# Kernel tuning notes

Hardware: AMD Instinct MI355X
Metric: run time of the kernel (lower is better)

Reference implementation:

```python
import jax, jax.numpy as jnp
import numpy as np

N_NODES = 50000
N_EDGES = 800000
DIM_IN = 128
DIM_H = 128
DIM_OUT = 8
N_GRAPHS = 32


def _glorot(key, shape):
    fan_in, fan_out = shape[0], shape[1]
    lim = float(np.sqrt(6.0 / (fan_in + fan_out)))
    return jax.random.uniform(key, shape, jnp.float32, -lim, lim)


def setup_inputs() -> dict:
    key = jax.random.key(0)
    ks = jax.random.split(key, 16)
    x = jax.random.normal(ks[0], (N_NODES, DIM_IN), jnp.float32)
    edge_index = jax.random.randint(ks[1], (2, N_EDGES), 0, N_NODES, jnp.int64)
    batch = jnp.sort(jax.random.randint(ks[2], (N_NODES,), 0, N_GRAPHS, jnp.int64))
    inp = {"x": x, "edge_index": edge_index, "batch": batch}
    # SAGEConv layers: lin_l (aggregated neighbors, with bias) + lin_r (self, no bias)
    dims = [(DIM_IN, DIM_H), (DIM_H, DIM_H), (DIM_H, DIM_H)]
    for i, (di, do) in enumerate(dims, start=1):
        inp[f"Wl{i}"] = _glorot(ks[2 + 3 * i], (di, do))
        inp[f"bl{i}"] = jnp.zeros((do,), jnp.float32)
        inp[f"Wr{i}"] = _glorot(ks[3 + 3 * i], (di, do))
    inp["W_lin1"] = _glorot(ks[13], (DIM_H, DIM_H))
    inp["b_lin1"] = jnp.zeros((DIM_H,), jnp.float32)
    inp["W_lin2"] = _glorot(ks[14], (DIM_H, DIM_OUT))
    inp["b_lin2"] = jnp.zeros((DIM_OUT,), jnp.float32)
    return inp


def _sage_conv(x, src, dst, Wl, bl, Wr):
    # mean aggregation of source-node features at destination nodes
    agg = jax.ops.segment_sum(x[src], dst, num_segments=N_NODES)
    cnt = jax.ops.segment_sum(jnp.ones((src.shape[0], 1), x.dtype), dst, num_segments=N_NODES)
    agg = agg / jnp.maximum(cnt, 1.0)
    return agg @ Wl + bl + x @ Wr


def reference(x, edge_index, batch, Wl1, bl1, Wr1, Wl2, bl2, Wr2, Wl3, bl3, Wr3,
              W_lin1, b_lin1, W_lin2, b_lin2):
    src, dst = edge_index[0], edge_index[1]
    h = jax.nn.relu(_sage_conv(x, src, dst, Wl1, bl1, Wr1))
    h = jax.nn.relu(_sage_conv(h, src, dst, Wl2, bl2, Wr2))
    h = jax.nn.relu(_sage_conv(h, src, dst, Wl3, bl3, Wr3))
    # global mean pool over graphs in the batch
    pooled = jax.ops.segment_sum(h, batch, num_segments=N_GRAPHS)
    gcnt = jax.ops.segment_sum(jnp.ones((h.shape[0], 1), h.dtype), batch, num_segments=N_GRAPHS)
    pooled = pooled / jnp.maximum(gcnt, 1.0)
    h = jax.nn.relu(pooled @ W_lin1 + b_lin1)
    # dropout p=0.5 is identity in eval mode
    return h @ W_lin2 + b_lin2
```

## Files before the change

kernel.cpp:

```cpp
#include <hip/hip_runtime.h>
#include <hip/hip_bf16.h>

#define N_NODES 50000
#define N_EDGES 800000
#define DIM 128
#define N_GRAPHS 32
#define POOL_ROWS 32
#define CAP 64
#define NPS 128
#define NSUP 391
#define SBCAP2 2432
#define EPB 8192
#define EPT 32
#define NBLK ((N_EDGES + EPB - 1) / EPB)

typedef _Float16 f16;
typedef __attribute__((ext_vector_type(2))) _Float16 f16x2;
typedef __attribute__((ext_vector_type(4))) _Float16 f16x4;
typedef __attribute__((ext_vector_type(8))) _Float16 f16x8;
typedef __attribute__((ext_vector_type(4))) float f32x4;

__global__ __launch_bounds__(256) void k_zero(float* __restrict__ pooled,
                                              int* __restrict__ gcnt,
                                              int* __restrict__ gCnt) {
  int i = blockIdx.x * 256 + threadIdx.x;
  if (i < N_GRAPHS * DIM) pooled[i] = 0.f;
  if (i < N_GRAPHS) gcnt[i] = 0;
  if (i < NSUP) gCnt[i] = 0;
}

__global__ __launch_bounds__(256) void k_part2(const int* __restrict__ src,
                                               const int* __restrict__ dst,
                                               int* __restrict__ gCnt,
                                               unsigned int* __restrict__ sbBuf) {
  __shared__ int hist[NSUP];
  __shared__ int base[NSUP];
  int tid = threadIdx.x;
  int e0 = blockIdx.x * EPB;
  int nE = min(EPB, N_EDGES - e0);
  for (int i = tid; i < NSUP; i += 256) hist[i] = 0;
  __syncthreads();
  unsigned pk[EPT];
  #pragma unroll
  for (int j = 0; j < EPT; ++j) {
    int idx = j * 256 + tid;
    if (idx < nE) {
      int e = e0 + idx;
      int d = dst[e], s = src[e];
      int sb = d >> 7;
      pk[j] = ((unsigned)sb << 23) | ((unsigned)(d & 127) << 16) | (unsigned)s;
      atomicAdd(&hist[sb], 1);
    } else pk[j] = 0xFFFFFFFFu;
  }
  __syncthreads();
  for (int i = tid; i < NSUP; i += 256) {
    int h = hist[i];
    base[i] = h ? atomicAdd(&gCnt[i], h) : 0;
    hist[i] = 0;
  }
  __syncthreads();
  #pragma unroll
  for (int j = 0; j < EPT; ++j) {
    unsigned p = pk[j];
    if (p != 0xFFFFFFFFu) {
      int sb = p >> 23;
      int slot = base[sb] + atomicAdd(&hist[sb], 1);
      if (slot < SBCAP2)
        sbBuf[(size_t)sb * SBCAP2 + slot] = p & 0x7FFFFFu;
    }
  }
}

__global__ __launch_bounds__(256) void k_bin(const int* __restrict__ gCnt,
                                             const unsigned int* __restrict__ sbBuf,
                                             int* __restrict__ cnt,
                                             unsigned short* __restrict__ esrc) {
  __shared__ unsigned short buck[NPS * CAP];
  __shared__ int cl[NPS];
  int sb = blockIdx.x, tid = threadIdx.x;
  for (int i = tid; i < NPS; i += 256) cl[i] = 0;
  __syncthreads();
  int n = min(gCnt[sb], SBCAP2);
  const unsigned int* buf = sbBuf + (size_t)sb * SBCAP2;
  for (int i = tid; i < n; i += 256) {
    unsigned p = buf[i];
    int dl = p >> 16;
    int slot = atomicAdd(&cl[dl], 1);
    if (slot < CAP) buck[dl * CAP + slot] = (unsigned short)(p & 0xFFFF);
  }
  __syncthreads();
  size_t basep = (size_t)sb * NPS * CAP;
  for (int i = tid; i < NPS * CAP; i += 256)
    esrc[basep + i] = buck[i];
  int n0 = sb * NPS;
  for (int d = tid; d < NPS; d += 256) {
    int node = n0 + d;
    if (node < N_NODES) cnt[node] = min(cl[d], CAP);
  }
}

__global__ void k_repack(const float* __restrict__ W0, const float* __restrict__ W1,
                         const float* __restrict__ W2, const float* __restrict__ W3,
                         const float* __restrict__ W4, const float* __restrict__ W5,
                         f16* __restrict__ pack) {
  int idx = blockIdx.x * 256 + threadIdx.x;
  if (idx >= 6 * 16384) return;
  int m = idx >> 14, r = idx & 16383;
  const float* W = m == 0 ? W0 : m == 1 ? W1 : m == 2 ? W2 : m == 3 ? W3 : m == 4 ? W4 : W5;
  int ct = r >> 11, ks = (r >> 9) & 3, l = (r >> 3) & 63, j = r & 7;
  int k = ks * 32 + ((l >> 4) << 3) + j;
  int c = ct * 16 + (l & 15);
  float w = W[k * DIM + c];
  f16 hi = (f16)w;
  f16 lo = (f16)(w - (float)hi);
  pack[m * 32768 + r] = hi;
  pack[m * 32768 + 16384 + r] = lo;
}

__global__ __launch_bounds__(256) void k_cvt(const float* __restrict__ in,
                                             f16* __restrict__ out) {
  int idx = blockIdx.x * 256 + threadIdx.x;
  if (idx >= N_NODES * DIM / 4) return;
  f32x4 v = *(const f32x4*)(in + idx * 4);
  f16x4 h;
  #pragma unroll
  for (int j = 0; j < 4; ++j) h[j] = (f16)v[j];
  *(f16x4*)(out + idx * 4) = h;
}

__global__ __launch_bounds__(256) void k_agg(const f16* __restrict__ H16,
                                             const int* __restrict__ cnt,
                                             const unsigned short* __restrict__ esrc,
                                             f16* __restrict__ agg16) {
  int node = blockIdx.x * 4 + (threadIdx.x >> 6);
  int lane = threadIdx.x & 63;
  int l16 = lane & 15;
  int sg = lane >> 4;
  int dcnt = cnt[node];
  int b = node * CAP, e = b + dcnt;

  f32x4 aA0 = (f32x4){0.f,0.f,0.f,0.f}, aA1 = aA0, aB0 = aA0, aB1 = aA0,
        aC0 = aA0, aC1 = aA0, aD0 = aA0, aD1 = aA0;
  int i = b + sg;
  for (; i + 12 < e; i += 16) {
    int s0 = esrc[i], s1 = esrc[i + 4], s2 = esrc[i + 8], s3 = esrc[i + 12];
    f16x8 v0 = *(const f16x8*)(H16 + (size_t)s0 * DIM + l16 * 8);
    f16x8 v1 = *(const f16x8*)(H16 + (size_t)s1 * DIM + l16 * 8);
    f16x8 v2 = *(const f16x8*)(H16 + (size_t)s2 * DIM + l16 * 8);
    f16x8 v3 = *(const f16x8*)(H16 + (size_t)s3 * DIM + l16 * 8);
    #pragma unroll
    for (int j = 0; j < 4; ++j) {
      aA0[j] += (float)v0[j]; aA1[j] += (float)v0[4 + j];
      aB0[j] += (float)v1[j]; aB1[j] += (float)v1[4 + j];
      aC0[j] += (float)v2[j]; aC1[j] += (float)v2[4 + j];
      aD0[j] += (float)v3[j]; aD1[j] += (float)v3[4 + j];
    }
  }
  for (; i < e; i += 4) {
    int s = esrc[i];
    f16x8 v = *(const f16x8*)(H16 + (size_t)s * DIM + l16 * 8);
    #pragma unroll
    for (int j = 0; j < 4; ++j) { aA0[j] += (float)v[j]; aA1[j] += (float)v[4 + j]; }
  }
  #pragma unroll
  for (int j = 0; j < 4; ++j) {
    aA0[j] = (aA0[j] + aB0[j]) + (aC0[j] + aD0[j]);
    aA1[j] = (aA1[j] + aB1[j]) + (aC1[j] + aD1[j]);
  }
  #pragma unroll
  for (int j = 0; j < 4; ++j) {
    aA0[j] += __shfl_xor(aA0[j], 16, 64);
    aA1[j] += __shfl_xor(aA1[j], 16, 64);
    aA0[j] += __shfl_xor(aA0[j], 32, 64);
    aA1[j] += __shfl_xor(aA1[j], 32, 64);
  }
  if (lane < 16) {
    float inv = 1.0f / (float)max(dcnt, 1);
    f16x8 r;
    #pragma unroll
    for (int j = 0; j < 4; ++j) {
      r[j] = (f16)(aA0[j] * inv);
      r[4 + j] = (f16)(aA1[j] * inv);
    }
    *(f16x8*)(agg16 + (size_t)node * DIM + l16 * 8) = r;
  }
}

__global__ __launch_bounds__(256) void k_gemm(const f16* __restrict__ Agg16,
                                              const f16* __restrict__ Hprev16,
                                              const f16* __restrict__ packWl,
                                              const f16* __restrict__ packWr,
                                              const float* __restrict__ bias,
                                              f16* __restrict__ Hout16) {
  __shared__ f16 wlds[32768];
  int tid = threadIdx.x;
  int wid = tid >> 6, l = tid & 63;
  int row0 = blockIdx.x * 64 + wid * 16;
  int arow = row0 + (l & 15);
  int arowc = min(arow, N_NODES - 1);
  int koff = (l >> 4) << 3;

  f32x4 acc[8];
  #pragma unroll
  for (int ct = 0; ct < 8; ++ct) acc[ct] = (f32x4){0.f, 0.f, 0.f, 0.f};

  #pragma unroll
  for (int mat = 0; mat < 2; ++mat) {
    const f16* A = (mat ? Hprev16 : Agg16) + (size_t)arowc * DIM + koff;
    f16x8 aa[4];
    #pragma unroll
    for (int ks = 0; ks < 4; ++ks) aa[ks] = *(const f16x8*)(A + ks * 32);

    const f16* P = mat ? packWr : packWl;
    if (mat) __syncthreads();
    #pragma unroll
    for (int it = 0; it < 16; ++it) {
      int idx = (it * 256 + tid) * 8;
      *(f16x8*)&wlds[idx] = *(const f16x8*)&P[idx];
    }
    __syncthreads();

    #pragma unroll
    for (int ct = 0; ct < 8; ++ct) {
      #pragma unroll
      for (int ks = 0; ks < 4; ++ks) {
        f16x8 bhi = *(const f16x8*)&wlds[((ct * 4 + ks) * 64 + l) * 8];
        f16x8 blo = *(const f16x8*)&wlds[16384 + ((ct * 4 + ks) * 64 + l) * 8];
        acc[ct] = __builtin_amdgcn_mfma_f32_16x16x32_f16(aa[ks], bhi, acc[ct], 0, 0, 0);
        acc[ct] = __builtin_amdgcn_mfma_f32_16x16x32_f16(aa[ks], blo, acc[ct], 0, 0, 0);
      }
    }
  }

  int drowb = row0 + ((l >> 4) << 2);
  int c0 = l & 15;
  #pragma unroll
  for (int ct = 0; ct < 8; ++ct) {
    int c = ct * 16 + c0;
    float bb = bias[c];
    #pragma unroll
    for (int i = 0; i < 4; ++i) {
      int r = drowb + i;
      if (r < N_NODES) {
        float v = acc[ct][i] + bb;
        v = v > 0.f ? v : 0.f;
        Hout16[(size_t)r * DIM + c] = (f16)v;
      }
    }
  }
}

__global__ __launch_bounds__(64) void k_pool(const f16* __restrict__ H16,
                                             const int* __restrict__ batch,
                                             float* __restrict__ pooled,
                                             int* __restrict__ gcnt) {
  int n0 = blockIdx.x * POOL_ROWS;
  int n1 = min(n0 + POOL_ROWS, N_NODES);
  int d = threadIdx.x;
  int g = batch[n0];
  float r0 = 0.f, r1 = 0.f;
  int c = 0;
  for (int n = n0; n < n1; ++n) {
    int gn = batch[n];
    if (gn != g) {
      atomicAdd(&pooled[g * DIM + d * 2], r0);
      atomicAdd(&pooled[g * DIM + d * 2 + 1], r1);
      if (d == 0) atomicAdd(&gcnt[g], c);
      r0 = r1 = 0.f; c = 0; g = gn;
    }
    f16x2 v = *(const f16x2*)(H16 + (size_t)n * DIM + d * 2);
    r0 += (float)v[0]; r1 += (float)v[1];
    c++;
  }
  atomicAdd(&pooled[g * DIM + d * 2], r0);
  atomicAdd(&pooled[g * DIM + d * 2 + 1], r1);
  if (d == 0) atomicAdd(&gcnt[g], c);
}

__global__ __launch_bounds__(128) void k_mlp(const float* __restrict__ pooled,
                                             const int* __restrict__ gcnt,
                                             const float* __restrict__ W1,
                                             const float* __restrict__ b1,
                                             const float* __restrict__ W2,
                                             const float* __restrict__ b2,
                                             float* __restrict__ out) {
  int g = blockIdx.x, c = threadIdx.x;
  __shared__ float pn[DIM];
  __shared__ float h1[DIM];
  pn[c] = pooled[g * DIM + c] / (float)max(gcnt[g], 1);
  __syncthreads();
  float s = b1[c];
  #pragma unroll 8
  for (int k = 0; k < DIM; ++k) s += pn[k] * W1[k * DIM + c];
  h1[c] = s > 0.f ? s : 0.f;
  __syncthreads();
  if (c < 8) {
    float s2 = b2[c];
    #pragma unroll 8
    for (int k = 0; k < DIM; ++k) s2 += h1[k] * W2[k * 8 + c];
    out[g * 8 + c] = s2;
  }
}

extern "C" void kernel_launch(void* const* d_in, const int* in_sizes, int n_in,
                              void* d_out, int out_size, void* d_ws, size_t ws_size,
                              hipStream_t stream) {
  const float* x = (const float*)d_in[0];
  const int* ei = (const int*)d_in[1];
  const int* src = ei;
  const int* dst = ei + N_EDGES;
  const int* batch = (const int*)d_in[2];
  const float* Wl1 = (const float*)d_in[3];  const float* bl1 = (const float*)d_in[4];  const float* Wr1 = (const float*)d_in[5];
  const float* Wl2 = (const float*)d_in[6];  const float* bl2 = (const float*)d_in[7];  const float* Wr2 = (const float*)d_in[8];
  const float* Wl3 = (const float*)d_in[9];  const float* bl3 = (const float*)d_in[10]; const float* Wr3 = (const float*)d_in[11];
  const float* W_1 = (const float*)d_in[12]; const float* b_1 = (const float*)d_in[13];
  const float* W_2 = (const float*)d_in[14]; const float* b_2 = (const float*)d_in[15];

  char* ws = (char*)d_ws;
  size_t off = 0;
  auto alloc = [&](size_t bytes) {
    void* p = ws + off;
    off += (bytes + 255) & ~(size_t)255;
    return p;
  };
  f16* agg16 = (f16*)alloc((size_t)N_NODES * DIM * 2);
  f16* h16A  = (f16*)alloc((size_t)N_NODES * DIM * 2);
  f16* h16B  = (f16*)alloc((size_t)N_NODES * DIM * 2);
  int* cnt   = (int*)alloc(N_NODES * 4);
  unsigned short* esrc = (unsigned short*)alloc((size_t)NSUP * NPS * CAP * 2);
  unsigned int* sbBuf  = (unsigned int*)alloc((size_t)NSUP * SBCAP2 * 4);
  f16* pack  = (f16*)alloc(6 * 32768 * sizeof(f16));
  float* pooled = (float*)alloc(N_GRAPHS * DIM * 4);
  int* gcnt = (int*)alloc(N_GRAPHS * 4);
  int* gCnt = (int*)alloc(NSUP * 4);

  k_zero<<<(N_GRAPHS * DIM + 255) / 256, 256, 0, stream>>>(pooled, gcnt, gCnt);
  k_part2<<<NBLK, 256, 0, stream>>>(src, dst, gCnt, sbBuf);
  k_repack<<<(6 * 16384 + 255) / 256, 256, 0, stream>>>(Wl1, Wr1, Wl2, Wr2, Wl3, Wr3, pack);
  k_cvt<<<(N_NODES * DIM / 4 + 255) / 256, 256, 0, stream>>>(x, h16A);
  k_bin<<<NSUP, 256, 0, stream>>>(gCnt, sbBuf, cnt, esrc);

  const int gemmBlocks = (N_NODES + 63) / 64;
  const int aggBlocks = N_NODES / 4;
  k_agg<<<aggBlocks, 256, 0, stream>>>(h16A, cnt, esrc, agg16);
  k_gemm<<<gemmBlocks, 256, 0, stream>>>(agg16, h16A, pack + 0 * 32768, pack + 1 * 32768, bl1, h16B);
  k_agg<<<aggBlocks, 256, 0, stream>>>(h16B, cnt, esrc, agg16);
  k_gemm<<<gemmBlocks, 256, 0, stream>>>(agg16, h16B, pack + 2 * 32768, pack + 3 * 32768, bl2, h16A);
  k_agg<<<aggBlocks, 256, 0, stream>>>(h16A, cnt, esrc, agg16);
  k_gemm<<<gemmBlocks, 256, 0, stream>>>(agg16, h16A, pack + 4 * 32768, pack + 5 * 32768, bl3, h16B);

  k_pool<<<(N_NODES + POOL_ROWS - 1) / POOL_ROWS, 64, 0, stream>>>(h16B, batch, pooled, gcnt);
  k_mlp<<<N_GRAPHS, 128, 0, stream>>>(pooled, gcnt, W_1, b_1, W_2, b_2, (float*)d_out);
}
```

Before: 254.5 us.

## Fuse neighbor mean aggregation into the SAGE GEMM kernel via LDS

Replaces the separate aggregation and GEMM kernels with one kernel per layer. Each wave gathers and averages neighbor features for its 16 rows into shared memory, then runs the MFMA GEMM on those rows and the self rows, streaming the four weight slices through LDS. This removes the global write and read of the aggregated matrix and two launches per layer. In exchange, gather parallelism drops sharply because each wave now processes 16 nodes in sequence and far fewer blocks are launched, so less memory latency is hidden.

```diff
diff --git a/kernel.cpp b/kernel.cpp
--- a/kernel.cpp
+++ b/kernel.cpp
@@ -13,6 +13,7 @@
 #define EPB 8192
 #define EPT 32
 #define NBLK ((N_EDGES + EPB - 1) / EPB)
+#define GBLK ((N_NODES + 63) / 64)
 
 typedef _Float16 f16;
 typedef __attribute__((ext_vector_type(2))) _Float16 f16x2;
@@ -128,115 +129,120 @@
   *(f16x4*)(out + idx * 4) = h;
 }
 
-__global__ __launch_bounds__(256) void k_agg(const f16* __restrict__ H16,
-                                             const int* __restrict__ cnt,
-                                             const unsigned short* __restrict__ esrc,
-                                             f16* __restrict__ agg16) {
-  int node = blockIdx.x * 4 + (threadIdx.x >> 6);
-  int lane = threadIdx.x & 63;
-  int l16 = lane & 15;
-  int sg = lane >> 4;
-  int dcnt = cnt[node];
-  int b = node * CAP, e = b + dcnt;
-
-  f32x4 aA0 = (f32x4){0.f,0.f,0.f,0.f}, aA1 = aA0, aB0 = aA0, aB1 = aA0,
-        aC0 = aA0, aC1 = aA0, aD0 = aA0, aD1 = aA0;
-  int i = b + sg;
-  for (; i + 12 < e; i += 16) {
-    int s0 = esrc[i], s1 = esrc[i + 4], s2 = esrc[i + 8], s3 = esrc[i + 12];
-    f16x8 v0 = *(const f16x8*)(H16 + (size_t)s0 * DIM + l16 * 8);
-    f16x8 v1 = *(const f16x8*)(H16 + (size_t)s1 * DIM + l16 * 8);
-    f16x8 v2 = *(const f16x8*)(H16 + (size_t)s2 * DIM + l16 * 8);
-    f16x8 v3 = *(const f16x8*)(H16 + (size_t)s3 * DIM + l16 * 8);
-    #pragma unroll
-    for (int j = 0; j < 4; ++j) {
-      aA0[j] += (float)v0[j]; aA1[j] += (float)v0[4 + j];
-      aB0[j] += (float)v1[j]; aB1[j] += (float)v1[4 + j];
-      aC0[j] += (float)v2[j]; aC1[j] += (float)v2[4 + j];
-      aD0[j] += (float)v3[j]; aD1[j] += (float)v3[4 + j];
-    }
-  }
-  for (; i < e; i += 4) {
-    int s = esrc[i];
-    f16x8 v = *(const f16x8*)(H16 + (size_t)s * DIM + l16 * 8);
-    #pragma unroll
-    for (int j = 0; j < 4; ++j) { aA0[j] += (float)v[j]; aA1[j] += (float)v[4 + j]; }
-  }
-  #pragma unroll
-  for (int j = 0; j < 4; ++j) {
-    aA0[j] = (aA0[j] + aB0[j]) + (aC0[j] + aD0[j]);
-    aA1[j] = (aA1[j] + aB1[j]) + (aC1[j] + aD1[j]);
-  }
-  #pragma unroll
-  for (int j = 0; j < 4; ++j) {
-    aA0[j] += __shfl_xor(aA0[j], 16, 64);
-    aA1[j] += __shfl_xor(aA1[j], 16, 64);
-    aA0[j] += __shfl_xor(aA0[j], 32, 64);
-    aA1[j] += __shfl_xor(aA1[j], 32, 64);
-  }
-  if (lane < 16) {
-    float inv = 1.0f / (float)max(dcnt, 1);
-    f16x8 r;
-    #pragma unroll
-    for (int j = 0; j < 4; ++j) {
-      r[j] = (f16)(aA0[j] * inv);
-      r[4 + j] = (f16)(aA1[j] * inv);
-    }
-    *(f16x8*)(agg16 + (size_t)node * DIM + l16 * 8) = r;
-  }
-}
-
-__global__ __launch_bounds__(256) void k_gemm(const f16* __restrict__ Agg16,
-                                              const f16* __restrict__ Hprev16,
-                                              const f16* __restrict__ packWl,
-                                              const f16* __restrict__ packWr,
-                                              const float* __restrict__ bias,
-                                              f16* __restrict__ Hout16) {
-  __shared__ f16 wlds[32768];
+__global__ __launch_bounds__(256) void k_fused(const f16* __restrict__ H16,
+                                               const int* __restrict__ cnt,
+                                               const unsigned short* __restrict__ esrc,
+                                               const f16* __restrict__ packL,
+                                               const float* __restrict__ bias,
+                                               f16* __restrict__ Hout16) {
+  __shared__ f16 wlds[16384];
+  __shared__ f16 aggl[64 * DIM];
   int tid = threadIdx.x;
   int wid = tid >> 6, l = tid & 63;
-  int row0 = blockIdx.x * 64 + wid * 16;
-  int arow = row0 + (l & 15);
-  int arowc = min(arow, N_NODES - 1);
-  int koff = (l >> 4) << 3;
+  int row0 = blockIdx.x * 64;
+  int row0w = row0 + wid * 16;
+  int l16 = l & 15;
+  int sg = l >> 4;
+
+  for (int it = 0; it < 16; ++it) {
+    int node = row0w + it;
+    f32x4 aA0 = (f32x4){0.f,0.f,0.f,0.f}, aA1 = aA0, aB0 = aA0, aB1 = aA0,
+          aC0 = aA0, aC1 = aA0, aD0 = aA0, aD1 = aA0;
+    int dcnt = 0;
+    if (node < N_NODES) {
+      dcnt = cnt[node];
+      int b = node * CAP, e = b + dcnt;
+      int i = b + sg;
+      for (; i + 12 < e; i += 16) {
+        int s0 = esrc[i], s1 = esrc[i + 4], s2 = esrc[i + 8], s3 = esrc[i + 12];
+        f16x8 v0 = *(const f16x8*)(H16 + (size_t)s0 * DIM + l16 * 8);
+        f16x8 v1 = *(const f16x8*)(H16 + (size_t)s1 * DIM + l16 * 8);
+        f16x8 v2 = *(const f16x8*)(H16 + (size_t)s2 * DIM + l16 * 8);
+        f16x8 v3 = *(const f16x8*)(H16 + (size_t)s3 * DIM + l16 * 8);
+        #pragma unroll
+        for (int j = 0; j < 4; ++j) {
+          aA0[j] += (float)v0[j]; aA1[j] += (float)v0[4 + j];
+          aB0[j] += (float)v1[j]; aB1[j] += (float)v1[4 + j];
+          aC0[j] += (float)v2[j]; aC1[j] += (float)v2[4 + j];
+          aD0[j] += (float)v3[j]; aD1[j] += (float)v3[4 + j];
+        }
+      }
+      for (; i < e; i += 4) {
+        int s = esrc[i];
+        f16x8 v = *(const f16x8*)(H16 + (size_t)s * DIM + l16 * 8);
+        #pragma unroll
+        for (int j = 0; j < 4; ++j) { aA0[j] += (float)v[j]; aA1[j] += (float)v[4 + j]; }
+      }
+    }
+    #pragma unroll
+    for (int j = 0; j < 4; ++j) {
+      aA0[j] = (aA0[j] + aB0[j]) + (aC0[j] + aD0[j]);
+      aA1[j] = (aA1[j] + aB1[j]) + (aC1[j] + aD1[j]);
+    }
+    #pragma unroll
+    for (int j = 0; j < 4; ++j) {
+      aA0[j] += __shfl_xor(aA0[j], 16, 64);
+      aA1[j] += __shfl_xor(aA1[j], 16, 64);
+      aA0[j] += __shfl_xor(aA0[j], 32, 64);
+      aA1[j] += __shfl_xor(aA1[j], 32, 64);
+    }
+    if (l < 16) {
+      float inv = 1.0f / (float)max(dcnt, 1);
+      f16x8 r;
+      #pragma unroll
+      for (int j = 0; j < 4; ++j) {
+        r[j] = (f16)(aA0[j] * inv);
+        r[4 + j] = (f16)(aA1[j] * inv);
+      }
+      *(f16x8*)&aggl[(wid * 16 + it) * DIM + l16 * 8] = r;
+    }
+  }
+
+  int arowc = min(row0w + l16, N_NODES - 1);
+  int koff = sg << 3;
+  f16x8 sa[4];
+  #pragma unroll
+  for (int ks = 0; ks < 4; ++ks)
+    sa[ks] = *(const f16x8*)(H16 + (size_t)arowc * DIM + koff + ks * 32);
+
+  __syncthreads();
+
+  f16x8 na[4];
+  #pragma unroll
+  for (int ks = 0; ks < 4; ++ks)
+    na[ks] = *(const f16x8*)&aggl[(wid * 16 + l16) * DIM + koff + ks * 32];
 
   f32x4 acc[8];
   #pragma unroll
   for (int ct = 0; ct < 8; ++ct) acc[ct] = (f32x4){0.f, 0.f, 0.f, 0.f};
 
   #pragma unroll
-  for (int mat = 0; mat < 2; ++mat) {
-    const f16* A = (mat ? Hprev16 : Agg16) + (size_t)arowc * DIM + koff;
-    f16x8 aa[4];
-    #pragma unroll
-    for (int ks = 0; ks < 4; ++ks) aa[ks] = *(const f16x8*)(A + ks * 32);
-
-    const f16* P = mat ? packWr : packWl;
-    if (mat) __syncthreads();
-    #pragma unroll
-    for (int it = 0; it < 16; ++it) {
-      int idx = (it * 256 + tid) * 8;
+  for (int ph = 0; ph < 4; ++ph) {
+    const f16* P = packL + ph * 16384;
+    __syncthreads();
+    #pragma unroll
+    for (int itr = 0; itr < 8; ++itr) {
+      int idx = (itr * 256 + tid) * 8;
       *(f16x8*)&wlds[idx] = *(const f16x8*)&P[idx];
     }
     __syncthreads();
-
     #pragma unroll
     for (int ct = 0; ct < 8; ++ct) {
       #pragma unroll
       for (int ks = 0; ks < 4; ++ks) {
-        f16x8 bhi = *(const f16x8*)&wlds[((ct * 4 + ks) * 64 + l) * 8];
-        f16x8 blo = *(const f16x8*)&wlds[16384 + ((ct * 4 + ks) * 64 + l) * 8];
-        acc[ct] = __builtin_amdgcn_mfma_f32_16x16x32_f16(aa[ks], bhi, acc[ct], 0, 0, 0);
-        acc[ct] = __builtin_amdgcn_mfma_f32_16x16x32_f16(aa[ks], blo, acc[ct], 0, 0, 0);
-      }
-    }
-  }
-
-  int drowb = row0 + ((l >> 4) << 2);
-  int c0 = l & 15;
+        f16x8 bfrag = *(const f16x8*)&wlds[((ct * 4 + ks) * 64 + l) * 8];
+        if (ph < 2)
+          acc[ct] = __builtin_amdgcn_mfma_f32_16x16x32_f16(na[ks], bfrag, acc[ct], 0, 0, 0);
+        else
+          acc[ct] = __builtin_amdgcn_mfma_f32_16x16x32_f16(sa[ks], bfrag, acc[ct], 0, 0, 0);
+      }
+    }
+  }
+
+  int drowb = row0 + wid * 16 + (sg << 2);
   #pragma unroll
   for (int ct = 0; ct < 8; ++ct) {
-    int c = ct * 16 + c0;
+    int c = ct * 16 + l16;
     float bb = bias[c];
     #pragma unroll
     for (int i = 0; i < 4; ++i) {
@@ -323,7 +329,6 @@
     off += (bytes + 255) & ~(size_t)255;
     return p;
   };
-  f16* agg16 = (f16*)alloc((size_t)N_NODES * DIM * 2);
   f16* h16A  = (f16*)alloc((size_t)N_NODES * DIM * 2);
   f16* h16B  = (f16*)alloc((size_t)N_NODES * DIM * 2);
   int* cnt   = (int*)alloc(N_NODES * 4);
@@ -340,14 +345,9 @@
   k_cvt<<<(N_NODES * DIM / 4 + 255) / 256, 256, 0, stream>>>(x, h16A);
   k_bin<<<NSUP, 256, 0, stream>>>(gCnt, sbBuf, cnt, esrc);
 
-  const int gemmBlocks = (N_NODES + 63) / 64;
-  const int aggBlocks = N_NODES / 4;
-  k_agg<<<aggBlocks, 256, 0, stream>>>(h16A, cnt, esrc, agg16);
-  k_gemm<<<gemmBlocks, 256, 0, stream>>>(agg16, h16A, pack + 0 * 32768, pack + 1 * 32768, bl1, h16B);
-  k_agg<<<aggBlocks, 256, 0, stream>>>(h16B, cnt, esrc, agg16);
-  k_gemm<<<gemmBlocks, 256, 0, stream>>>(agg16, h16B, pack + 2 * 32768, pack + 3 * 32768, bl2, h16A);
-  k_agg<<<aggBlocks, 256, 0, stream>>>(h16A, cnt, esrc, agg16);
-  k_gemm<<<gemmBlocks, 256, 0, stream>>>(agg16, h16A, pack + 4 * 32768, pack + 5 * 32768, bl3, h16B);
+  k_fused<<<GBLK, 256, 0, stream>>>(h16A, cnt, esrc, pack + 0 * 65536, bl1, h16B);
+  k_fused<<<GBLK, 256, 0, stream>>>(h16B, cnt, esrc, pack + 1 * 65536, bl2, h16A);
+  k_fused<<<GBLK, 256, 0, stream>>>(h16A, cnt, esrc, pack + 2 * 65536, bl3, h16B);
 
   k_pool<<<(N_NODES + POOL_ROWS - 1) / POOL_ROWS, 64, 0, stream>>>(h16B, batch, pooled, gcnt);
   k_mlp<<<N_GRAPHS, 128, 0, stream>>>(pooled, gcnt, W_1, b_1, W_2, b_2, (float*)d_out);
```

Result: slower. 360.5 us (+41.6%).
